# Kernel optimization log

Measured on AMD Instinct MI355X. Metric: run time of the kernel, lower is better.

## Reference

```python
import jax, jax.numpy as jnp
import numpy as np

N_STEPS = 64
B, H, W, C = 16, 128, 128, 16
T = 8          # n_time_points
HID = 128      # hidden_size
FC0_IN = 3 * C + 1  # perceive concat + time-progress channel


def setup_inputs() -> dict:
    key = jax.random.key(0)
    ks = jax.random.split(key, 8)
    inputs = jax.random.normal(ks[0], (B, H, W, C), dtype=jnp.float32)
    acquire_at_step = jnp.sort(jax.random.randint(ks[1], (B, T), 0, N_STEPS), axis=-1)
    # depthwise 3x3 kernels in HWIO layout (I = C/groups = 1)
    p0_w = jax.random.normal(ks[2], (3, 3, 1, C), dtype=jnp.float32) * 0.1
    p0_b = jax.random.normal(ks[3], (C,), dtype=jnp.float32) * 0.1
    p1_w = jax.random.normal(ks[4], (3, 3, 1, C), dtype=jnp.float32) * 0.1
    p1_b = jax.random.normal(ks[5], (C,), dtype=jnp.float32) * 0.1
    fc0_w = jax.random.normal(ks[6], (HID, FC0_IN), dtype=jnp.float32) * (1.0 / np.sqrt(FC0_IN))
    fc0_b = jnp.zeros((HID,), dtype=jnp.float32)
    fc1_w = jax.random.normal(ks[7], (C, HID), dtype=jnp.float32) * (1.0 / np.sqrt(HID))
    return {"inputs": inputs, "acquire_at_step": acquire_at_step,
            "p0_w": p0_w, "p0_b": p0_b, "p1_w": p1_w, "p1_b": p1_b,
            "fc0_w": fc0_w, "fc0_b": fc0_b, "fc1_w": fc1_w}


def _dwconv(x, w, b):
    # depthwise 3x3, stride 1, reflect padding 1 (NHWC)
    xp = jnp.pad(x, ((0, 0), (1, 1), (1, 1), (0, 0)), mode='reflect')
    y = jax.lax.conv_general_dilated(
        xp, w, window_strides=(1, 1), padding='VALID',
        dimension_numbers=('NHWC', 'HWIO', 'NHWC'),
        feature_group_count=C)
    return y + b


def reference(inputs, acquire_at_step, p0_w, p0_b, p1_w, p1_b, fc0_w, fc0_b, fc1_w):
    dtype = inputs.dtype

    def step_fn(carry, step):
        x, data = carry
        # perceive: identity + two depthwise convs, concat on channel dim
        z1 = _dwconv(x, p0_w, p0_b)
        z2 = _dwconv(x, p1_w, p1_b)
        y = jnp.concatenate([x, z1, z2], axis=-1)            # [B,H,W,3C]
        prog = jnp.full((B, H, W, 1), 0.0, dtype) + (step.astype(dtype) / N_STEPS)
        y = jnp.concatenate([y, prog], axis=-1)              # [B,H,W,3C+1]
        # 2-layer MLP per cell
        h = jax.nn.relu(jnp.einsum('bhwc,kc->bhwk', y, fc0_w) + fc0_b)
        dx = jax.nn.sigmoid(jnp.einsum('bhwk,ck->bhwc', h, fc1_w))
        # fire_rate == 1.0 -> no stochastic masking; residual update
        x = x + dx
        # acquire snapshot wherever acquire_at_step == step (only step > 0)
        mask = (acquire_at_step == step) & (step > 0)        # [B,T]
        data = jnp.where(mask[:, :, None, None, None], x[:, None], data)
        return (x, data), None

    data0 = jnp.zeros((B, T, H, W, C), dtype)
    (_, data), _ = jax.lax.scan(step_fn, (inputs, data0), jnp.arange(N_STEPS))
    return data
```

## Files before the change

kernel.cpp:

```cpp
#include <hip/hip_runtime.h>
#include <hip/hip_bf16.h>

constexpr int B = 16, H = 128, W = 128, C = 16, T = 8, HID = 128, NSTEPS = 64;

using f32x4  = __attribute__((ext_vector_type(4))) float;
using bf16x8 = __attribute__((ext_vector_type(8))) short;

__device__ __forceinline__ unsigned short bf16_hi(float v) {
    __hip_bfloat16 h = __float2bfloat16(v);
    return *reinterpret_cast<unsigned short*>(&h);
}
__device__ __forceinline__ float bf16_f32(unsigned short u) {
    union { unsigned int u; float f; } c; c.u = ((unsigned int)u) << 16; return c.f;
}

__global__ void prep_pack(const float* __restrict__ fc0_w, const float* __restrict__ fc1_w,
                          unsigned short* __restrict__ pack) {
    for (int e = threadIdx.x; e < 40 * 64; e += 256) {
        const int row = e >> 6, l = e & 63;
        const int m = l & 15, g = l >> 4;
        unsigned short v[8];
        if (row < 32) {
            const int nt = row >> 2, f = row & 3;
            const int n = nt * 16 + m;
            const int kbase = ((f >= 2) ? 32 : 0) + g * 8;
            #pragma unroll
            for (int j = 0; j < 8; ++j) {
                const int k = kbase + j;
                const float x = (k < 49) ? fc0_w[n * 49 + k] : 0.0f;
                const unsigned short hi = bf16_hi(x);
                v[j] = (f & 1) ? bf16_hi(x - bf16_f32(hi)) : hi;
            }
        } else {
            const int rr = row - 32, ks = rr >> 1, f = rr & 1;
            #pragma unroll
            for (int j = 0; j < 8; ++j) {
                const float x = fc1_w[m * HID + ks * 32 + g * 8 + j];
                const unsigned short hi = bf16_hi(x);
                v[j] = f ? bf16_hi(x - bf16_f32(hi)) : hi;
            }
        }
        #pragma unroll
        for (int j = 0; j < 8; ++j) pack[e * 8 + j] = v[j];
    }
}

__global__ void zero_acq0(const int* __restrict__ acq, float* __restrict__ out) {
    const int bt = blockIdx.x;
    if (acq[bt] != 0) return;
    float4* p = reinterpret_cast<float4*>(out + (size_t)bt * (H * W * C));
    for (int i = threadIdx.x; i < (H * W * C) / 4; i += 256)
        p[i] = make_float4(0.0f, 0.0f, 0.0f, 0.0f);
}

__global__ __launch_bounds__(256, 2) void nca_step(
    const float* __restrict__ x_in, float* __restrict__ x_out,
    const float* __restrict__ p0_w, const float* __restrict__ p0_b,
    const float* __restrict__ p1_w, const float* __restrict__ p1_b,
    const unsigned short* __restrict__ pack, const float* __restrict__ fc0_b,
    const int* __restrict__ acq, float* __restrict__ out, int step)
{
    __shared__ float wlds[32 * 256];
    __shared__ float hlds[4 * 2048];

    const int tid  = threadIdx.x;
    const int wv   = tid >> 6;
    const int lane = tid & 63;
    const int m    = lane & 15;
    const int g    = lane >> 4;

    #pragma unroll
    for (int e0 = 0; e0 < 2048; e0 += 256) {
        const int e = e0 + tid;
        const int4 v = *reinterpret_cast<const int4*>(pack + (size_t)e * 8);
        *reinterpret_cast<int4*>(&wlds[e * 4]) = v;
    }

    const int blockbase = blockIdx.x * 256;
    const int b = blockbase >> 14;

    int snapmask = 0;
    if (step > 0) {
        #pragma unroll
        for (int t = 0; t < T; ++t)
            snapmask |= (acq[b * T + t] == step) ? (1 << t) : 0;
    }
    bf16x8 w1f[8];
    #pragma unroll
    for (int q = 0; q < 8; ++q)
        w1f[q] = *reinterpret_cast<const bf16x8*>(pack + ((32 + q) * 64 + lane) * 8);
    float bias[8];
    #pragma unroll
    for (int nt = 0; nt < 8; ++nt) bias[nt] = fc0_b[nt * 16 + m];

    const float prog = (float)step * (1.0f / (float)NSTEPS);
    const float* pw = (g >= 2) ? p0_w : p1_w;
    const float* pb = (g >= 2) ? p0_b : p1_b;
    const int ch = (g & 1) * 8;
    float* hb = hlds + (wv << 11);
    const int lb = lane << 2;
    const int m7 = m & 7;

    for (int t = 0; t < 4; ++t) {
        const int cellbase = blockbase + t * 64 + wv * 16;
        const int hrow  = (cellbase >> 7) & (H - 1);
        const int wbase = cellbase & (W - 1);
        const int wcol  = wbase + m;

        float z[8], xcen[8];
        #pragma unroll
        for (int j = 0; j < 8; ++j) z[j] = pb[ch + j];
        #pragma unroll
        for (int di = -1; di <= 1; ++di) {
            int hh = hrow + di; hh = (hh < 0) ? 1 : ((hh > H - 1) ? H - 2 : hh);
            #pragma unroll
            for (int dj = -1; dj <= 1; ++dj) {
                int ww = wcol + dj; ww = (ww < 0) ? 1 : ((ww > W - 1) ? W - 2 : ww);
                const float4* p4 = reinterpret_cast<const float4*>(
                    x_in + (((size_t)(b * H + hh) * W + ww) << 4) + ch);
                const float4 q0 = p4[0], q1 = p4[1];
                const float xv[8] = {q0.x, q0.y, q0.z, q0.w, q1.x, q1.y, q1.z, q1.w};
                const int tap = (di + 1) * 3 + (dj + 1);
                #pragma unroll
                for (int j = 0; j < 8; ++j)
                    z[j] = fmaf(xv[j], pw[tap * 16 + ch + j], z[j]);
                if (di == 0 && dj == 0) {
                    #pragma unroll
                    for (int j = 0; j < 8; ++j) xcen[j] = xv[j];
                }
            }
        }

        const float4 xold4 = *reinterpret_cast<const float4*>(
            x_in + ((size_t)(cellbase + m) << 4) + g * 4);

        bf16x8 a0h, a0l, a1h, a1l;
        #pragma unroll
        for (int j = 0; j < 8; ++j) {
            const float f0 = (g < 2) ? xcen[j] : z[j];
            const float f1 = (g < 2) ? z[j] : ((g == 2 && j == 0) ? prog : 0.0f);
            const unsigned short h0 = bf16_hi(f0);
            a0h[j] = (short)h0;  a0l[j] = (short)bf16_hi(f0 - bf16_f32(h0));
            const unsigned short h1 = bf16_hi(f1);
            a1h[j] = (short)h1;  a1l[j] = (short)bf16_hi(f1 - bf16_f32(h1));
        }

        if (t == 0) __syncthreads();

        #pragma unroll
        for (int nt = 0; nt < 8; ++nt) {
            const int rb = nt << 10;
            const bf16x8 b0h = *reinterpret_cast<const bf16x8*>(&wlds[rb + lb]);
            const bf16x8 b0l = *reinterpret_cast<const bf16x8*>(&wlds[rb + 256 + lb]);
            const bf16x8 b1h = *reinterpret_cast<const bf16x8*>(&wlds[rb + 512 + lb]);
            const bf16x8 b1l = *reinterpret_cast<const bf16x8*>(&wlds[rb + 768 + lb]);
            f32x4 acc = {0.0f, 0.0f, 0.0f, 0.0f};
            acc = __builtin_amdgcn_mfma_f32_16x16x32_bf16(a0h, b0h, acc, 0, 0, 0);
            acc = __builtin_amdgcn_mfma_f32_16x16x32_bf16(a0l, b0h, acc, 0, 0, 0);
            acc = __builtin_amdgcn_mfma_f32_16x16x32_bf16(a0h, b0l, acc, 0, 0, 0);
            acc = __builtin_amdgcn_mfma_f32_16x16x32_bf16(a1h, b1h, acc, 0, 0, 0);
            acc = __builtin_amdgcn_mfma_f32_16x16x32_bf16(a1l, b1h, acc, 0, 0, 0);
            acc = __builtin_amdgcn_mfma_f32_16x16x32_bf16(a1h, b1l, acc, 0, 0, 0);
            const int hid4 = (nt << 2) + (m >> 2), ml = m & 3;
            #pragma unroll
            for (int r = 0; r < 4; ++r) {
                const int cr = g * 4 + r;
                hb[cr * 128 + (((hid4 ^ (cr & 7)) << 2) | ml)] = fmaxf(acc[r] + bias[nt], 0.0f);
            }
        }

        f32x4 acc2 = {0.0f, 0.0f, 0.0f, 0.0f};
        #pragma unroll
        for (int ks = 0; ks < 4; ++ks) {
            const float4 h0 = *reinterpret_cast<const float4*>(
                &hb[m * 128 + ((((ks << 3) + (g << 1) + 0) ^ m7) << 2)]);
            const float4 h1 = *reinterpret_cast<const float4*>(
                &hb[m * 128 + ((((ks << 3) + (g << 1) + 1) ^ m7) << 2)]);
            const float hv[8] = {h0.x, h0.y, h0.z, h0.w, h1.x, h1.y, h1.z, h1.w};
            bf16x8 bh, bl;
            #pragma unroll
            for (int j = 0; j < 8; ++j) {
                const unsigned short hi = bf16_hi(hv[j]);
                bh[j] = (short)hi;
                bl[j] = (short)bf16_hi(hv[j] - bf16_f32(hi));
            }
            acc2 = __builtin_amdgcn_mfma_f32_16x16x32_bf16(w1f[ks * 2 + 0], bh, acc2, 0, 0, 0);
            acc2 = __builtin_amdgcn_mfma_f32_16x16x32_bf16(w1f[ks * 2 + 1], bh, acc2, 0, 0, 0);
            acc2 = __builtin_amdgcn_mfma_f32_16x16x32_bf16(w1f[ks * 2 + 0], bl, acc2, 0, 0, 0);
        }

        const size_t cell = (size_t)(cellbase + m);
        float4 xn;
        xn.x = xold4.x + 1.0f / (1.0f + __expf(-acc2[0]));
        xn.y = xold4.y + 1.0f / (1.0f + __expf(-acc2[1]));
        xn.z = xold4.z + 1.0f / (1.0f + __expf(-acc2[2]));
        xn.w = xold4.w + 1.0f / (1.0f + __expf(-acc2[3]));
        *reinterpret_cast<float4*>(x_out + (cell << 4) + g * 4) = xn;
        if (snapmask) {
            #pragma unroll
            for (int tt = 0; tt < T; ++tt) {
                if (snapmask & (1 << tt)) {
                    *reinterpret_cast<float4*>(out + (size_t)(b * T + tt) * (H * W * C)
                        + (((size_t)hrow * W + wbase + m) << 4) + g * 4) = xn;
                }
            }
        }
    }
}

extern "C" void kernel_launch(void* const* d_in, const int* in_sizes, int n_in,
                              void* d_out, int out_size, void* d_ws, size_t ws_size,
                              hipStream_t stream) {
    const float* inputs = (const float*)d_in[0];
    const int*   acq    = (const int*)d_in[1];
    const float* p0_w   = (const float*)d_in[2];
    const float* p0_b   = (const float*)d_in[3];
    const float* p1_w   = (const float*)d_in[4];
    const float* p1_b   = (const float*)d_in[5];
    const float* fc0_w  = (const float*)d_in[6];
    const float* fc0_b  = (const float*)d_in[7];
    const float* fc1_w  = (const float*)d_in[8];
    float* out = (float*)d_out;

    const size_t state_elems = (size_t)B * H * W * C;
    float* bufA = (float*)d_ws;
    float* bufB = bufA + state_elems;
    unsigned short* pack = (unsigned short*)(bufB + state_elems);

    zero_acq0<<<B * T, 256, 0, stream>>>(acq, out);
    prep_pack<<<1, 256, 0, stream>>>(fc0_w, fc1_w, pack);

    const int n_cells = B * H * W;
    const dim3 grid(n_cells / 256), block(256);

    const float* xin = inputs;
    for (int step = 0; step < NSTEPS; ++step) {
        float* xout = (step & 1) ? bufB : bufA;
        nca_step<<<grid, block, 0, stream>>>(
            xin, xout, p0_w, p0_b, p1_w, p1_b,
            pack, fc0_b, acq, out, step);
        xin = xout;
    }
}
```

Measured before the change: 2.104 ms.

## Prefetch next tile's conv taps and split MFMA accumulators for ILP

Global loads of the 9 conv taps and the residual input for the next tile are issued into double-buffered registers before the MFMA work of the current tile, hiding global memory latency behind compute. The MFMA chains in both layers are split into two independent accumulators that are summed at the end, which shortens dependent MFMA chains. The cost is higher register pressure from the double-buffered float4 arrays, which may reduce occupancy, and a small change in floating-point summation order.

```diff
diff --git a/kernel.cpp b/kernel.cpp
--- a/kernel.cpp
+++ b/kernel.cpp
@@ -79,60 +79,80 @@
     const int blockbase = blockIdx.x * 256;
     const int b = blockbase >> 14;
 
-    int snapmask = 0;
-    if (step > 0) {
-        #pragma unroll
-        for (int t = 0; t < T; ++t)
-            snapmask |= (acq[b * T + t] == step) ? (1 << t) : 0;
-    }
-    bf16x8 w1f[8];
-    #pragma unroll
-    for (int q = 0; q < 8; ++q)
-        w1f[q] = *reinterpret_cast<const bf16x8*>(pack + ((32 + q) * 64 + lane) * 8);
-    float bias[8];
-    #pragma unroll
-    for (int nt = 0; nt < 8; ++nt) bias[nt] = fc0_b[nt * 16 + m];
-
-    const float prog = (float)step * (1.0f / (float)NSTEPS);
     const float* pw = (g >= 2) ? p0_w : p1_w;
     const float* pb = (g >= 2) ? p0_b : p1_b;
     const int ch = (g & 1) * 8;
     float* hb = hlds + (wv << 11);
     const int lb = lane << 2;
     const int m7 = m & 7;
-
+    const float prog = (float)step * (1.0f / (float)NSTEPS);
+
+    int snapmask = 0;
+    if (step > 0) {
+        #pragma unroll
+        for (int t = 0; t < T; ++t)
+            snapmask |= (acq[b * T + t] == step) ? (1 << t) : 0;
+    }
+    bf16x8 w1f[8];
+    #pragma unroll
+    for (int q = 0; q < 8; ++q)
+        w1f[q] = *reinterpret_cast<const bf16x8*>(pack + ((32 + q) * 64 + lane) * 8);
+    float bias[8];
+    #pragma unroll
+    for (int nt = 0; nt < 8; ++nt) bias[nt] = fc0_b[nt * 16 + m];
+
+    float4 cva[2][9], cvb[2][9], xo4[2];
+
+    auto issue_tile = [&](int tt) {
+        const int par = tt & 1;
+        const int cb = blockbase + tt * 64 + wv * 16;
+        const int hr = (cb >> 7) & (H - 1);
+        const int wb = cb & (W - 1);
+        const int wc = wb + m;
+        int hs[3], ws[3];
+        hs[0] = (hr == 0) ? 1 : hr - 1;  hs[1] = hr;  hs[2] = (hr == H - 1) ? H - 2 : hr + 1;
+        ws[0] = (wc == 0) ? 1 : wc - 1;  ws[1] = wc;  ws[2] = (wc == W - 1) ? W - 2 : wc + 1;
+        #pragma unroll
+        for (int i = 0; i < 3; ++i) {
+            #pragma unroll
+            for (int j = 0; j < 3; ++j) {
+                const float4* p4 = reinterpret_cast<const float4*>(
+                    x_in + (((size_t)(b * H + hs[i]) * W + ws[j]) << 4) + ch);
+                cva[par][i * 3 + j] = p4[0];
+                cvb[par][i * 3 + j] = p4[1];
+            }
+        }
+        xo4[par] = *reinterpret_cast<const float4*>(
+            x_in + ((size_t)(cb + m) << 4) + (g << 2));
+    };
+
+    issue_tile(0);
+
+    #pragma unroll
     for (int t = 0; t < 4; ++t) {
+        const int par = t & 1;
         const int cellbase = blockbase + t * 64 + wv * 16;
         const int hrow  = (cellbase >> 7) & (H - 1);
         const int wbase = cellbase & (W - 1);
-        const int wcol  = wbase + m;
 
         float z[8], xcen[8];
         #pragma unroll
         for (int j = 0; j < 8; ++j) z[j] = pb[ch + j];
         #pragma unroll
-        for (int di = -1; di <= 1; ++di) {
-            int hh = hrow + di; hh = (hh < 0) ? 1 : ((hh > H - 1) ? H - 2 : hh);
-            #pragma unroll
-            for (int dj = -1; dj <= 1; ++dj) {
-                int ww = wcol + dj; ww = (ww < 0) ? 1 : ((ww > W - 1) ? W - 2 : ww);
-                const float4* p4 = reinterpret_cast<const float4*>(
-                    x_in + (((size_t)(b * H + hh) * W + ww) << 4) + ch);
-                const float4 q0 = p4[0], q1 = p4[1];
-                const float xv[8] = {q0.x, q0.y, q0.z, q0.w, q1.x, q1.y, q1.z, q1.w};
-                const int tap = (di + 1) * 3 + (dj + 1);
+        for (int p = 0; p < 9; ++p) {
+            const float4 qa = cva[par][p], qb = cvb[par][p];
+            const float xv[8] = {qa.x, qa.y, qa.z, qa.w, qb.x, qb.y, qb.z, qb.w};
+            #pragma unroll
+            for (int j = 0; j < 8; ++j)
+                z[j] = fmaf(xv[j], pw[p * 16 + ch + j], z[j]);
+            if (p == 4) {
                 #pragma unroll
-                for (int j = 0; j < 8; ++j)
-                    z[j] = fmaf(xv[j], pw[tap * 16 + ch + j], z[j]);
-                if (di == 0 && dj == 0) {
-                    #pragma unroll
-                    for (int j = 0; j < 8; ++j) xcen[j] = xv[j];
-                }
-            }
-        }
-
-        const float4 xold4 = *reinterpret_cast<const float4*>(
-            x_in + ((size_t)(cellbase + m) << 4) + g * 4);
+                for (int j = 0; j < 8; ++j) xcen[j] = xv[j];
+            }
+        }
+        const float4 xold4 = xo4[par];
+
+        if (t < 3) issue_tile(t + 1);
 
         bf16x8 a0h, a0l, a1h, a1l;
         #pragma unroll
@@ -154,22 +174,25 @@
             const bf16x8 b0l = *reinterpret_cast<const bf16x8*>(&wlds[rb + 256 + lb]);
             const bf16x8 b1h = *reinterpret_cast<const bf16x8*>(&wlds[rb + 512 + lb]);
             const bf16x8 b1l = *reinterpret_cast<const bf16x8*>(&wlds[rb + 768 + lb]);
-            f32x4 acc = {0.0f, 0.0f, 0.0f, 0.0f};
-            acc = __builtin_amdgcn_mfma_f32_16x16x32_bf16(a0h, b0h, acc, 0, 0, 0);
-            acc = __builtin_amdgcn_mfma_f32_16x16x32_bf16(a0l, b0h, acc, 0, 0, 0);
-            acc = __builtin_amdgcn_mfma_f32_16x16x32_bf16(a0h, b0l, acc, 0, 0, 0);
-            acc = __builtin_amdgcn_mfma_f32_16x16x32_bf16(a1h, b1h, acc, 0, 0, 0);
-            acc = __builtin_amdgcn_mfma_f32_16x16x32_bf16(a1l, b1h, acc, 0, 0, 0);
-            acc = __builtin_amdgcn_mfma_f32_16x16x32_bf16(a1h, b1l, acc, 0, 0, 0);
+            f32x4 accL = {0.0f, 0.0f, 0.0f, 0.0f};
+            f32x4 accH = {0.0f, 0.0f, 0.0f, 0.0f};
+            accL = __builtin_amdgcn_mfma_f32_16x16x32_bf16(a0h, b0h, accL, 0, 0, 0);
+            accH = __builtin_amdgcn_mfma_f32_16x16x32_bf16(a1h, b1h, accH, 0, 0, 0);
+            accL = __builtin_amdgcn_mfma_f32_16x16x32_bf16(a0l, b0h, accL, 0, 0, 0);
+            accH = __builtin_amdgcn_mfma_f32_16x16x32_bf16(a1l, b1h, accH, 0, 0, 0);
+            accL = __builtin_amdgcn_mfma_f32_16x16x32_bf16(a0h, b0l, accL, 0, 0, 0);
+            accH = __builtin_amdgcn_mfma_f32_16x16x32_bf16(a1h, b1l, accH, 0, 0, 0);
             const int hid4 = (nt << 2) + (m >> 2), ml = m & 3;
             #pragma unroll
             for (int r = 0; r < 4; ++r) {
                 const int cr = g * 4 + r;
-                hb[cr * 128 + (((hid4 ^ (cr & 7)) << 2) | ml)] = fmaxf(acc[r] + bias[nt], 0.0f);
-            }
-        }
-
-        f32x4 acc2 = {0.0f, 0.0f, 0.0f, 0.0f};
+                hb[cr * 128 + (((hid4 ^ (cr & 7)) << 2) | ml)] =
+                    fmaxf(accL[r] + accH[r] + bias[nt], 0.0f);
+            }
+        }
+
+        f32x4 acc2a = {0.0f, 0.0f, 0.0f, 0.0f};
+        f32x4 acc2b = {0.0f, 0.0f, 0.0f, 0.0f};
         #pragma unroll
         for (int ks = 0; ks < 4; ++ks) {
             const float4 h0 = *reinterpret_cast<const float4*>(
@@ -184,6 +207,7 @@
                 bh[j] = (short)hi;
                 bl[j] = (short)bf16_hi(hv[j] - bf16_f32(hi));
             }
+            f32x4& acc2 = (ks & 1) ? acc2b : acc2a;
             acc2 = __builtin_amdgcn_mfma_f32_16x16x32_bf16(w1f[ks * 2 + 0], bh, acc2, 0, 0, 0);
             acc2 = __builtin_amdgcn_mfma_f32_16x16x32_bf16(w1f[ks * 2 + 1], bh, acc2, 0, 0, 0);
             acc2 = __builtin_amdgcn_mfma_f32_16x16x32_bf16(w1f[ks * 2 + 0], bl, acc2, 0, 0, 0);
@@ -191,10 +215,10 @@
 
         const size_t cell = (size_t)(cellbase + m);
         float4 xn;
-        xn.x = xold4.x + 1.0f / (1.0f + __expf(-acc2[0]));
-        xn.y = xold4.y + 1.0f / (1.0f + __expf(-acc2[1]));
-        xn.z = xold4.z + 1.0f / (1.0f + __expf(-acc2[2]));
-        xn.w = xold4.w + 1.0f / (1.0f + __expf(-acc2[3]));
+        xn.x = xold4.x + 1.0f / (1.0f + __expf(-(acc2a[0] + acc2b[0])));
+        xn.y = xold4.y + 1.0f / (1.0f + __expf(-(acc2a[1] + acc2b[1])));
+        xn.z = xold4.z + 1.0f / (1.0f + __expf(-(acc2a[2] + acc2b[2])));
+        xn.w = xold4.w + 1.0f / (1.0f + __expf(-(acc2a[3] + acc2b[3])));
         *reinterpret_cast<float4*>(x_out + (cell << 4) + g * 4) = xn;
         if (snapmask) {
             #pragma unroll
```

Result: slower. 3.554 ms (+68.9%).

## Remap blocks to 4-row strips with rolling row window and prefetch

Applied to the files above, without the earlier changes.

Each block now handles a 64-column by 4-row strip, so each wave walks down 4 rows of one column segment instead of 4 segments of a single row. The stencil keeps a rolling 3-row register window, so each new row costs one fresh row of loads instead of nine tap loads. The next row and the next residual value are prefetched before the MFMA work of the current row to hide global latency. The cost is extra register pressure from holding four row buffers, which could reduce occupancy.

```diff
diff --git a/kernel.cpp b/kernel.cpp
--- a/kernel.cpp
+++ b/kernel.cpp
@@ -76,8 +76,21 @@
         *reinterpret_cast<int4*>(&wlds[e * 4]) = v;
     }
 
-    const int blockbase = blockIdx.x * 256;
-    const int b = blockbase >> 14;
+    const int bid = blockIdx.x;
+    const int b   = bid >> 6;
+    const int ib  = bid & 63;
+    const int rb  = ib >> 1;
+    const int c0  = (ib & 1) * 64 + wv * 16;
+    const int wc  = c0 + m;
+
+    const float* pw = (g >= 2) ? p0_w : p1_w;
+    const float* pb = (g >= 2) ? p0_b : p1_b;
+    const int ch = (g & 1) * 8;
+    float* hb = hlds + (wv << 11);
+    const int lb = lane << 2;
+    const int m7 = m & 7;
+    const float prog = (float)step * (1.0f / (float)NSTEPS);
+    const size_t imgbase = (size_t)b * (H * W);
 
     int snapmask = 0;
     if (step > 0) {
@@ -93,46 +106,84 @@
     #pragma unroll
     for (int nt = 0; nt < 8; ++nt) bias[nt] = fc0_b[nt * 16 + m];
 
-    const float prog = (float)step * (1.0f / (float)NSTEPS);
-    const float* pw = (g >= 2) ? p0_w : p1_w;
-    const float* pb = (g >= 2) ? p0_b : p1_b;
-    const int ch = (g & 1) * 8;
-    float* hb = hlds + (wv << 11);
-    const int lb = lane << 2;
-    const int m7 = m & 7;
-
+    int ws[3];
+    ws[0] = (wc == 0) ? 1 : wc - 1;  ws[1] = wc;  ws[2] = (wc == W - 1) ? W - 2 : wc + 1;
+
+    const int r0 = rb * 4;
+    float4 rA[3][2], rB[3][2], rC[3][2], rN[3][2];
+    {
+        const int rm1 = (r0 == 0) ? 1 : r0 - 1;
+        #pragma unroll
+        for (int j = 0; j < 3; ++j) {
+            const float4* p = reinterpret_cast<const float4*>(
+                x_in + ((imgbase + (size_t)rm1 * W + ws[j]) << 4) + ch);
+            rA[j][0] = p[0]; rA[j][1] = p[1];
+        }
+        #pragma unroll
+        for (int j = 0; j < 3; ++j) {
+            const float4* p = reinterpret_cast<const float4*>(
+                x_in + ((imgbase + (size_t)r0 * W + ws[j]) << 4) + ch);
+            rB[j][0] = p[0]; rB[j][1] = p[1];
+        }
+        #pragma unroll
+        for (int j = 0; j < 3; ++j) {
+            const float4* p = reinterpret_cast<const float4*>(
+                x_in + ((imgbase + (size_t)(r0 + 1) * W + ws[j]) << 4) + ch);
+            rC[j][0] = p[0]; rC[j][1] = p[1];
+        }
+    }
+    float4 xold4 = *reinterpret_cast<const float4*>(
+        x_in + ((imgbase + (size_t)r0 * W + wc) << 4) + (g << 2));
+    float4 xoldN;
+
+    #pragma unroll
     for (int t = 0; t < 4; ++t) {
-        const int cellbase = blockbase + t * 64 + wv * 16;
-        const int hrow  = (cellbase >> 7) & (H - 1);
-        const int wbase = cellbase & (W - 1);
-        const int wcol  = wbase + m;
+        const int r = r0 + t;
 
         float z[8], xcen[8];
         #pragma unroll
         for (int j = 0; j < 8; ++j) z[j] = pb[ch + j];
         #pragma unroll
-        for (int di = -1; di <= 1; ++di) {
-            int hh = hrow + di; hh = (hh < 0) ? 1 : ((hh > H - 1) ? H - 2 : hh);
-            #pragma unroll
-            for (int dj = -1; dj <= 1; ++dj) {
-                int ww = wcol + dj; ww = (ww < 0) ? 1 : ((ww > W - 1) ? W - 2 : ww);
-                const float4* p4 = reinterpret_cast<const float4*>(
-                    x_in + (((size_t)(b * H + hh) * W + ww) << 4) + ch);
-                const float4 q0 = p4[0], q1 = p4[1];
-                const float xv[8] = {q0.x, q0.y, q0.z, q0.w, q1.x, q1.y, q1.z, q1.w};
-                const int tap = (di + 1) * 3 + (dj + 1);
-                #pragma unroll
-                for (int j = 0; j < 8; ++j)
-                    z[j] = fmaf(xv[j], pw[tap * 16 + ch + j], z[j]);
-                if (di == 0 && dj == 0) {
-                    #pragma unroll
-                    for (int j = 0; j < 8; ++j) xcen[j] = xv[j];
-                }
-            }
-        }
-
-        const float4 xold4 = *reinterpret_cast<const float4*>(
-            x_in + ((size_t)(cellbase + m) << 4) + g * 4);
+        for (int j = 0; j < 3; ++j) {
+            const float4 qa = rA[j][0], qb = rA[j][1];
+            const float xv[8] = {qa.x, qa.y, qa.z, qa.w, qb.x, qb.y, qb.z, qb.w};
+            #pragma unroll
+            for (int jj = 0; jj < 8; ++jj)
+                z[jj] = fmaf(xv[jj], pw[j * 16 + ch + jj], z[jj]);
+        }
+        #pragma unroll
+        for (int j = 0; j < 3; ++j) {
+            const float4 qa = rB[j][0], qb = rB[j][1];
+            const float xv[8] = {qa.x, qa.y, qa.z, qa.w, qb.x, qb.y, qb.z, qb.w};
+            #pragma unroll
+            for (int jj = 0; jj < 8; ++jj)
+                z[jj] = fmaf(xv[jj], pw[(3 + j) * 16 + ch + jj], z[jj]);
+        }
+        #pragma unroll
+        for (int j = 0; j < 3; ++j) {
+            const float4 qa = rC[j][0], qb = rC[j][1];
+            const float xv[8] = {qa.x, qa.y, qa.z, qa.w, qb.x, qb.y, qb.z, qb.w};
+            #pragma unroll
+            for (int jj = 0; jj < 8; ++jj)
+                z[jj] = fmaf(xv[jj], pw[(6 + j) * 16 + ch + jj], z[jj]);
+        }
+        {
+            const float4 qa = rB[1][0], qb = rB[1][1];
+            xcen[0] = qa.x; xcen[1] = qa.y; xcen[2] = qa.z; xcen[3] = qa.w;
+            xcen[4] = qb.x; xcen[5] = qb.y; xcen[6] = qb.z; xcen[7] = qb.w;
+        }
+
+        if (t < 3) {
+            int rt2 = r + 2; if (rt2 > H - 1) rt2 = H - 2;
+            #pragma unroll
+            for (int j = 0; j < 3; ++j) {
+                const float4* p = reinterpret_cast<const float4*>(
+                    x_in + ((imgbase + (size_t)rt2 * W + ws[j]) << 4) + ch);
+                rN[j][0] = p[0]; rN[j][1] = p[1];
+            }
+            xoldN = *reinterpret_cast<const float4*>(
+                x_in + ((imgbase + (size_t)(r + 1) * W + wc) << 4) + (g << 2));
+        }
 
         bf16x8 a0h, a0l, a1h, a1l;
         #pragma unroll
@@ -149,11 +200,11 @@
 
         #pragma unroll
         for (int nt = 0; nt < 8; ++nt) {
-            const int rb = nt << 10;
-            const bf16x8 b0h = *reinterpret_cast<const bf16x8*>(&wlds[rb + lb]);
-            const bf16x8 b0l = *reinterpret_cast<const bf16x8*>(&wlds[rb + 256 + lb]);
-            const bf16x8 b1h = *reinterpret_cast<const bf16x8*>(&wlds[rb + 512 + lb]);
-            const bf16x8 b1l = *reinterpret_cast<const bf16x8*>(&wlds[rb + 768 + lb]);
+            const int rbo = nt << 10;
+            const bf16x8 b0h = *reinterpret_cast<const bf16x8*>(&wlds[rbo + lb]);
+            const bf16x8 b0l = *reinterpret_cast<const bf16x8*>(&wlds[rbo + 256 + lb]);
+            const bf16x8 b1h = *reinterpret_cast<const bf16x8*>(&wlds[rbo + 512 + lb]);
+            const bf16x8 b1l = *reinterpret_cast<const bf16x8*>(&wlds[rbo + 768 + lb]);
             f32x4 acc = {0.0f, 0.0f, 0.0f, 0.0f};
             acc = __builtin_amdgcn_mfma_f32_16x16x32_bf16(a0h, b0h, acc, 0, 0, 0);
             acc = __builtin_amdgcn_mfma_f32_16x16x32_bf16(a0l, b0h, acc, 0, 0, 0);
@@ -163,9 +214,9 @@
             acc = __builtin_amdgcn_mfma_f32_16x16x32_bf16(a1h, b1l, acc, 0, 0, 0);
             const int hid4 = (nt << 2) + (m >> 2), ml = m & 3;
             #pragma unroll
-            for (int r = 0; r < 4; ++r) {
-                const int cr = g * 4 + r;
-                hb[cr * 128 + (((hid4 ^ (cr & 7)) << 2) | ml)] = fmaxf(acc[r] + bias[nt], 0.0f);
+            for (int rr = 0; rr < 4; ++rr) {
+                const int cr = g * 4 + rr;
+                hb[cr * 128 + (((hid4 ^ (cr & 7)) << 2) | ml)] = fmaxf(acc[rr] + bias[nt], 0.0f);
             }
         }
 
@@ -189,21 +240,31 @@
             acc2 = __builtin_amdgcn_mfma_f32_16x16x32_bf16(w1f[ks * 2 + 0], bl, acc2, 0, 0, 0);
         }
 
-        const size_t cell = (size_t)(cellbase + m);
+        const size_t cell = imgbase + (size_t)r * W + wc;
         float4 xn;
         xn.x = xold4.x + 1.0f / (1.0f + __expf(-acc2[0]));
         xn.y = xold4.y + 1.0f / (1.0f + __expf(-acc2[1]));
         xn.z = xold4.z + 1.0f / (1.0f + __expf(-acc2[2]));
         xn.w = xold4.w + 1.0f / (1.0f + __expf(-acc2[3]));
-        *reinterpret_cast<float4*>(x_out + (cell << 4) + g * 4) = xn;
+        *reinterpret_cast<float4*>(x_out + (cell << 4) + (g << 2)) = xn;
         if (snapmask) {
             #pragma unroll
             for (int tt = 0; tt < T; ++tt) {
                 if (snapmask & (1 << tt)) {
                     *reinterpret_cast<float4*>(out + (size_t)(b * T + tt) * (H * W * C)
-                        + (((size_t)hrow * W + wbase + m) << 4) + g * 4) = xn;
+                        + (((size_t)r * W + wc) << 4) + (g << 2)) = xn;
                 }
             }
+        }
+
+        if (t < 3) {
+            #pragma unroll
+            for (int j = 0; j < 3; ++j) {
+                rA[j][0] = rB[j][0]; rA[j][1] = rB[j][1];
+                rB[j][0] = rC[j][0]; rB[j][1] = rC[j][1];
+                rC[j][0] = rN[j][0]; rC[j][1] = rN[j][1];
+            }
+            xold4 = xoldN;
         }
     }
 }
```

Measured after the change: 2.207 ms. +4.9%, slower.
